# Optimization experiments

Hardware: AMD Instinct MI355X
Metric: run time of the kernel (lower is better)

The kernel has to match this reference:

```python
import jax, jax.numpy as jnp
import numpy as np

B, C, O = 16384, 128, 128


def setup_inputs() -> dict:
    key = jax.random.key(0)
    k1, k2, k3 = jax.random.split(key, 3)
    x = jax.random.normal(k1, (B, C, 3, 3), dtype=jnp.float32)
    # 9 stacked Conv2d(C, O, 3x3) weights/biases, position p = 3*r + c (row-major)
    W = jax.random.normal(k2, (9, O, C, 3, 3), dtype=jnp.float32) * 0.05
    b = jax.random.normal(k3, (9, O), dtype=jnp.float32) * 0.05
    return {"x": x, "W": W, "b": b}


def reference(x, W, b):
    Bn = x.shape[0]
    xr = x.reshape(Bn, C, 3, 3)
    # F.interpolate(scale_factor=3, mode='nearest'): each pixel replicated 3x3
    ins = jnp.repeat(jnp.repeat(xr, 3, axis=2), 3, axis=3)  # (B, C, 9, 9)
    # patch for output position (r, c) is ins[:, :, 2+r:5+r, 2+c:5+c]
    patches = jnp.stack(
        [ins[:, :, 2 + r:5 + r, 2 + c:5 + c] for r in range(3) for c in range(3)],
        axis=0,
    )  # (9, B, C, 3, 3)
    # each conv reduces its 3x3xC patch to one pixel per out-channel
    out = jnp.einsum('pbcij,pocij->bpo', patches, W) + b[None]  # (B, 9, O)
    out = out.transpose(0, 2, 1).reshape(Bn, O, 3, 3)  # row-major (r, c)
    return out
```

## Files before the change

kernel.cpp:

```cpp
#include <hip/hip_runtime.h>
#include <hip/hip_bf16.h>

typedef __bf16 bf16_t;
typedef __attribute__((ext_vector_type(8))) __bf16 bf16x8;
typedef __attribute__((ext_vector_type(4))) float f32x4;

#define KDIM 1152
#define NDIM 1152
#define BM 128
#define BN 288
#define BK 32
#define NIT 36
#define NTILES 4
#define A_STEP 8192
#define A_PANEL 294912
#define B_STEP 18432
#define B_TILE (36 * B_STEP)
#define CVT_BLOCKS 9216

__device__ __forceinline__ void gload_lds16(const void* g, void* l) {
    __builtin_amdgcn_global_load_lds(
        (const __attribute__((address_space(1))) void*)g,
        (__attribute__((address_space(3))) void*)l, 16, 0, 0);
}

__global__ void prep(const float* __restrict__ X, bf16_t* __restrict__ Xb,
                     const float* __restrict__ W, const float* __restrict__ bvec,
                     bf16_t* __restrict__ Bm, float* __restrict__ bias)
{
    __shared__ char L[4096];
    const int bid = blockIdx.x;
    const int tid = threadIdx.x;
    if (bid < CVT_BLOCKS) {
        const int wv = (bid << 2) + (tid >> 6);
        const int l = tid & 63;
        const int P = wv / 288;
        const int rem = wv - P * 288;
        const int T = rem >> 3;
        const int rb = rem & 7;
        const int row = P * 128 + rb * 16 + (l >> 2);
        const int k = T * 32 + (l & 3) * 8;
        const float* src = X + (size_t)row * KDIM + k;
        f32x4 lo = *(const f32x4*)src;
        f32x4 hi = *(const f32x4*)(src + 4);
        bf16x8 v;
        #pragma unroll
        for (int e = 0; e < 4; ++e) { v[e] = (__bf16)lo[e]; v[4 + e] = (__bf16)hi[e]; }
        char* wl = L + (tid >> 6) * 1024;
        *(bf16x8*)(wl + ((l & 3) * 16 + (l >> 2)) * 16) = v;
        __builtin_amdgcn_s_barrier();
        bf16x8 o = *(const bf16x8*)(wl + l * 16);
        *(bf16x8*)((char*)Xb + ((size_t)wv * 64 + l) * 16) = o;
        return;
    }
    const int t = (bid - CVT_BLOCKS) * 256 + tid;
    if (t < NDIM) {
        const int o = t / 9, p = t - o * 9;
        bias[t] = bvec[p * 128 + o];
    }
    const int c = t & 127;
    const int o = (t >> 7) & 127;
    const int p = t >> 14;
    if (p >= 9) return;
    const int r = p / 3, cc = p - r * 3;
    float eff[3][3] = {{0.f,0.f,0.f},{0.f,0.f,0.f},{0.f,0.f,0.f}};
    const float* w = W + (size_t)((p * 128 + o) * 128 + c) * 9;
    #pragma unroll
    for (int i = 0; i < 3; ++i) {
        const int a = (2 + r + i) / 3;
        #pragma unroll
        for (int j = 0; j < 3; ++j) {
            const int bb = (2 + cc + j) / 3;
            eff[a][bb] += w[i * 3 + j];
        }
    }
    const int n = o * 9 + p;
    const int tile = n / BN;
    const int nin = n - tile * BN;
    #pragma unroll
    for (int a = 0; a < 3; ++a)
        #pragma unroll
        for (int bb = 0; bb < 3; ++bb) {
            const int k = c * 9 + a * 3 + bb;
            const size_t idx = (size_t)tile * (B_TILE / 2)
                             + (k >> 5) * (B_STEP / 2)
                             + (nin >> 4) * 512 + ((k >> 3) & 3) * 128
                             + (nin & 15) * 8 + (k & 7);
            Bm[idx] = (bf16_t)eff[a][bb];
        }
}

__launch_bounds__(256, 2)
__global__ void ind_gemm(const bf16_t* __restrict__ Xb,
                         const bf16_t* __restrict__ Bm,
                         const float* __restrict__ bias,
                         float* __restrict__ out)
{
    __shared__ char As[2][A_STEP];
    __shared__ char Bs[2][B_STEP];
    __shared__ char Scrap[1024];

    const int tid = threadIdx.x;
    const int lane = tid & 63;
    const int wid = tid >> 6;
    const int wm = wid >> 1;
    const int wn = wid & 1;

    const int bid = blockIdx.x;
    const int swz = (bid & 7) * 64 + (bid >> 3);
    const int mt = swz >> 2;
    const int nt = swz & 3;
    const int m0 = mt * BM;

    const int fr = (lane >> 4) * 256 + (lane & 15) * 16;
    const char* apanel = (const char*)Xb + (size_t)mt * A_PANEL;
    const char* bpanel = (const char*)Bm + (size_t)nt * B_TILE;

    f32x4 acc[4][9];
    #pragma unroll
    for (int i = 0; i < 4; ++i)
        #pragma unroll
        for (int j = 0; j < 9; ++j)
            acc[i][j] = (f32x4){0.f, 0.f, 0.f, 0.f};

    bf16x8 af[4], bfr[9];

    #define GLD(T, BUF) do {                                                \
        const char* sa_ = apanel + (size_t)(T) * A_STEP;                    \
        gload_lds16(sa_ + tid * 16,        &As[BUF][tid * 16]);             \
        gload_lds16(sa_ + 4096 + tid * 16, &As[BUF][4096 + tid * 16]);      \
        const char* sb_ = bpanel + (size_t)(T) * B_STEP;                    \
        _Pragma("unroll")                                                   \
        for (int r_ = 0; r_ < 4; ++r_) {                                    \
            const int u_ = (tid + r_ * 256) * 16;                           \
            gload_lds16(sb_ + u_, &Bs[BUF][u_]);                            \
        }                                                                   \
        if (tid < 128) gload_lds16(sb_ + (1024 + tid) * 16,                 \
                                   &Bs[BUF][(1024 + tid) * 16]);            \
        else           gload_lds16(bpanel + tid * 16, Scrap);               \
    } while (0)

    #define RD(CUR) do {                                                    \
        _Pragma("unroll")                                                   \
        for (int mi_ = 0; mi_ < 4; ++mi_)                                   \
            af[mi_] = *(const bf16x8*)(&As[CUR][(wm * 4 + mi_) * 1024 + fr]); \
        _Pragma("unroll")                                                   \
        for (int j_ = 0; j_ < 9; ++j_)                                      \
            bfr[j_] = *(const bf16x8*)(&Bs[CUR][(wn * 9 + j_) * 1024 + fr]); \
        asm volatile("s_waitcnt lgkmcnt(0)" ::: "memory");                  \
        __builtin_amdgcn_sched_barrier(0);                                  \
        __builtin_amdgcn_s_barrier();                                       \
    } while (0)

    #define MFMA36() do {                                                   \
        __builtin_amdgcn_s_setprio(1);                                      \
        _Pragma("unroll")                                                   \
        for (int mi_ = 0; mi_ < 4; ++mi_)                                   \
            _Pragma("unroll")                                               \
            for (int j_ = 0; j_ < 9; ++j_)                                  \
                acc[mi_][j_] = __builtin_amdgcn_mfma_f32_16x16x32_bf16(     \
                    af[mi_], bfr[j_], acc[mi_][j_], 0, 0, 0);               \
        __builtin_amdgcn_s_setprio(0);                                      \
    } while (0)

    #define WAITV(N) do {                                                   \
        asm volatile("s_waitcnt vmcnt(" #N ")" ::: "memory");               \
        __builtin_amdgcn_sched_barrier(0);                                  \
    } while (0)

    GLD(0, 0);
    GLD(1, 1);
    WAITV(7);
    __builtin_amdgcn_s_barrier();

    #pragma unroll 1
    for (int t2 = 0; t2 < 17; ++t2) {
        const int t = 2 * t2;
        RD(0);
        GLD(t + 2, 0);
        MFMA36();
        WAITV(7);
        __builtin_amdgcn_s_barrier();
        RD(1);
        GLD(t + 3, 1);
        MFMA36();
        WAITV(7);
        __builtin_amdgcn_s_barrier();
    }
    RD(0);
    MFMA36();
    WAITV(0);
    __builtin_amdgcn_s_barrier();
    RD(1);
    MFMA36();

    #undef GLD
    #undef RD
    #undef MFMA36
    #undef WAITV

    const int orow = (lane >> 4) * 4;
    const int ocol = lane & 15;
    const int gn0 = nt * BN + wn * 144 + ocol;
    #pragma unroll
    for (int ni = 0; ni < 9; ++ni) {
        const float bv = bias[gn0 + ni * 16];
        #pragma unroll
        for (int mi = 0; mi < 4; ++mi) {
            float* po = out + (size_t)(m0 + wm * 64 + mi * 16 + orow) * NDIM
                            + gn0 + ni * 16;
            #pragma unroll
            for (int r = 0; r < 4; ++r)
                po[(size_t)r * NDIM] = acc[mi][ni][r] + bv;
        }
    }
}

extern "C" void kernel_launch(void* const* d_in, const int* in_sizes, int n_in,
                              void* d_out, int out_size, void* d_ws, size_t ws_size,
                              hipStream_t stream)
{
    const float* x  = (const float*)d_in[0];
    const float* W  = (const float*)d_in[1];
    const float* bv = (const float*)d_in[2];
    float* out = (float*)d_out;

    bf16_t* Xb   = (bf16_t*)d_ws;
    bf16_t* Bm   = (bf16_t*)((char*)d_ws + (size_t)16384 * KDIM * sizeof(bf16_t));
    float*  bias = (float*)((char*)Bm + (size_t)KDIM * NDIM * sizeof(bf16_t));

    prep<<<CVT_BLOCKS + 576, 256, 0, stream>>>(x, Xb, W, bv, Bm, bias);
    ind_gemm<<<512, 256, 0, stream>>>(Xb, Bm, bias, out);
}
```

Baseline: 79.98 us.

## Triple-buffer GEMM LDS stages and double work per prep convert block

The GEMM main loop moves from double to triple LDS buffering. Each iteration now issues the load for stage t+2 into a third slot before reading the current slot, and one of the two barriers per step is removed. This is meant to hide global-load latency and cut synchronisation. Separately, the bf16 convert blocks in prep each handle two 16x32 tiles per wave, halving the block count. The larger LDS footprint (about 79KB per block) may reduce occupancy under the two-blocks-per-CU launch bound.

```diff
diff --git a/kernel.cpp b/kernel.cpp
--- a/kernel.cpp
+++ b/kernel.cpp
@@ -16,7 +16,7 @@
 #define A_PANEL 294912
 #define B_STEP 18432
 #define B_TILE (36 * B_STEP)
-#define CVT_BLOCKS 9216
+#define CVT_BLOCKS 4608
 
 __device__ __forceinline__ void gload_lds16(const void* g, void* l) {
     __builtin_amdgcn_global_load_lds(
@@ -28,29 +28,50 @@
                      const float* __restrict__ W, const float* __restrict__ bvec,
                      bf16_t* __restrict__ Bm, float* __restrict__ bias)
 {
-    __shared__ char L[4096];
+    __shared__ char L[8192];
     const int bid = blockIdx.x;
     const int tid = threadIdx.x;
     if (bid < CVT_BLOCKS) {
-        const int wv = (bid << 2) + (tid >> 6);
+        const int gv = (bid << 3) + ((tid >> 6) << 1);
         const int l = tid & 63;
-        const int P = wv / 288;
-        const int rem = wv - P * 288;
-        const int T = rem >> 3;
-        const int rb = rem & 7;
-        const int row = P * 128 + rb * 16 + (l >> 2);
-        const int k = T * 32 + (l & 3) * 8;
-        const float* src = X + (size_t)row * KDIM + k;
-        f32x4 lo = *(const f32x4*)src;
-        f32x4 hi = *(const f32x4*)(src + 4);
-        bf16x8 v;
-        #pragma unroll
-        for (int e = 0; e < 4; ++e) { v[e] = (__bf16)lo[e]; v[4 + e] = (__bf16)hi[e]; }
-        char* wl = L + (tid >> 6) * 1024;
-        *(bf16x8*)(wl + ((l & 3) * 16 + (l >> 2)) * 16) = v;
+        char* wl = L + (tid >> 6) * 2048;
+        {
+            const int P = gv / 288;
+            const int rem = gv - P * 288;
+            const int T = rem >> 3;
+            const int rb = rem & 7;
+            const int row = P * 128 + rb * 16 + (l >> 2);
+            const int k = T * 32 + (l & 3) * 8;
+            const float* src = X + (size_t)row * KDIM + k;
+            f32x4 lo = *(const f32x4*)src;
+            f32x4 hi = *(const f32x4*)(src + 4);
+            bf16x8 v;
+            #pragma unroll
+            for (int e = 0; e < 4; ++e) { v[e] = (__bf16)lo[e]; v[4 + e] = (__bf16)hi[e]; }
+            *(bf16x8*)(wl + ((l & 3) * 16 + (l >> 2)) * 16) = v;
+        }
+        {
+            const int g1 = gv + 1;
+            const int P = g1 / 288;
+            const int rem = g1 - P * 288;
+            const int T = rem >> 3;
+            const int rb = rem & 7;
+            const int row = P * 128 + rb * 16 + (l >> 2);
+            const int k = T * 32 + (l & 3) * 8;
+            const float* src = X + (size_t)row * KDIM + k;
+            f32x4 lo = *(const f32x4*)src;
+            f32x4 hi = *(const f32x4*)(src + 4);
+            bf16x8 v;
+            #pragma unroll
+            for (int e = 0; e < 4; ++e) { v[e] = (__bf16)lo[e]; v[4 + e] = (__bf16)hi[e]; }
+            *(bf16x8*)(wl + 1024 + ((l & 3) * 16 + (l >> 2)) * 16) = v;
+        }
         __builtin_amdgcn_s_barrier();
-        bf16x8 o = *(const bf16x8*)(wl + l * 16);
-        *(bf16x8*)((char*)Xb + ((size_t)wv * 64 + l) * 16) = o;
+        bf16x8 o0 = *(const bf16x8*)(wl + l * 16);
+        bf16x8 o1 = *(const bf16x8*)(wl + 1024 + l * 16);
+        char* dst = (char*)Xb + (size_t)gv * 1024;
+        *(bf16x8*)(dst + l * 16) = o0;
+        *(bf16x8*)(dst + 1024 + l * 16) = o1;
         return;
     }
     const int t = (bid - CVT_BLOCKS) * 256 + tid;
@@ -96,8 +117,8 @@
                          const float* __restrict__ bias,
                          float* __restrict__ out)
 {
-    __shared__ char As[2][A_STEP];
-    __shared__ char Bs[2][B_STEP];
+    __shared__ char As[3][A_STEP];
+    __shared__ char Bs[3][B_STEP];
     __shared__ char Scrap[1024];
 
     const int tid = threadIdx.x;
@@ -125,31 +146,30 @@
 
     bf16x8 af[4], bfr[9];
 
-    #define GLD(T, BUF) do {                                                \
+    #define GLD(T, SLOT) do {                                               \
         const char* sa_ = apanel + (size_t)(T) * A_STEP;                    \
-        gload_lds16(sa_ + tid * 16,        &As[BUF][tid * 16]);             \
-        gload_lds16(sa_ + 4096 + tid * 16, &As[BUF][4096 + tid * 16]);      \
+        gload_lds16(sa_ + tid * 16,        &As[SLOT][tid * 16]);            \
+        gload_lds16(sa_ + 4096 + tid * 16, &As[SLOT][4096 + tid * 16]);     \
         const char* sb_ = bpanel + (size_t)(T) * B_STEP;                    \
         _Pragma("unroll")                                                   \
         for (int r_ = 0; r_ < 4; ++r_) {                                    \
             const int u_ = (tid + r_ * 256) * 16;                           \
-            gload_lds16(sb_ + u_, &Bs[BUF][u_]);                            \
+            gload_lds16(sb_ + u_, &Bs[SLOT][u_]);                           \
         }                                                                   \
         if (tid < 128) gload_lds16(sb_ + (1024 + tid) * 16,                 \
-                                   &Bs[BUF][(1024 + tid) * 16]);            \
+                                   &Bs[SLOT][(1024 + tid) * 16]);           \
         else           gload_lds16(bpanel + tid * 16, Scrap);               \
     } while (0)
 
-    #define RD(CUR) do {                                                    \
+    #define RD(SLOT) do {                                                   \
         _Pragma("unroll")                                                   \
         for (int mi_ = 0; mi_ < 4; ++mi_)                                   \
-            af[mi_] = *(const bf16x8*)(&As[CUR][(wm * 4 + mi_) * 1024 + fr]); \
+            af[mi_] = *(const bf16x8*)(&As[SLOT][(wm * 4 + mi_) * 1024 + fr]); \
         _Pragma("unroll")                                                   \
         for (int j_ = 0; j_ < 9; ++j_)                                      \
-            bfr[j_] = *(const bf16x8*)(&Bs[CUR][(wn * 9 + j_) * 1024 + fr]); \
+            bfr[j_] = *(const bf16x8*)(&Bs[SLOT][(wn * 9 + j_) * 1024 + fr]); \
         asm volatile("s_waitcnt lgkmcnt(0)" ::: "memory");                  \
         __builtin_amdgcn_sched_barrier(0);                                  \
-        __builtin_amdgcn_s_barrier();                                       \
     } while (0)
 
     #define MFMA36() do {                                                   \
@@ -168,36 +188,39 @@
         __builtin_amdgcn_sched_barrier(0);                                  \
     } while (0)
 
+    #define ITER(T, SLOT, SLOT2) do {                                       \
+        GLD((T) + 2, SLOT2);      \
+        RD(SLOT);                                                           \
+        MFMA36();                                                           \
+        WAITV(7);                      \
+        __builtin_amdgcn_s_barrier();                                       \
+    } while (0)
+
     GLD(0, 0);
     GLD(1, 1);
     WAITV(7);
     __builtin_amdgcn_s_barrier();
 
     #pragma unroll 1
-    for (int t2 = 0; t2 < 17; ++t2) {
-        const int t = 2 * t2;
-        RD(0);
-        GLD(t + 2, 0);
-        MFMA36();
-        WAITV(7);
-        __builtin_amdgcn_s_barrier();
-        RD(1);
-        GLD(t + 3, 1);
-        MFMA36();
-        WAITV(7);
-        __builtin_amdgcn_s_barrier();
-    }
-    RD(0);
+    for (int tt = 0; tt < 11; ++tt) {
+        const int t = 3 * tt;
+        ITER(t,     0, 2);
+        ITER(t + 1, 1, 0);
+        ITER(t + 2, 2, 1);
+    }
+    ITER(33, 0, 2);
+    RD(1);
     MFMA36();
     WAITV(0);
     __builtin_amdgcn_s_barrier();
-    RD(1);
+    RD(2);
     MFMA36();
 
     #undef GLD
     #undef RD
     #undef MFMA36
     #undef WAITV
+    #undef ITER
 
     const int orow = (lane >> 4) * 4;
     const int ocol = lane & 15;
```

After: 85.82 us. 1.07x slower.

## Fuse fp32-to-bf16 activation conversion into GEMM, loading raw fp32 tiles to LDS

Applied to the files above, without the earlier changes.

Removes the separate pass that converted X to bf16 into a tiled workspace layout. The GEMM now streams fp32 X rows directly into LDS with an XOR swizzle and converts to bf16 in registers just before the MFMAs. This saves a full write and re-read of the converted activation, but doubles the A-tile LDS footprint and global bytes the GEMM loads. It also adds conversion instructions to the MFMA loop.

```diff
diff --git a/kernel.cpp b/kernel.cpp
--- a/kernel.cpp
+++ b/kernel.cpp
@@ -12,11 +12,9 @@
 #define BK 32
 #define NIT 36
 #define NTILES 4
-#define A_STEP 8192
-#define A_PANEL 294912
+#define AF_STEP 16384
 #define B_STEP 18432
 #define B_TILE (36 * B_STEP)
-#define CVT_BLOCKS 9216
 
 __device__ __forceinline__ void gload_lds16(const void* g, void* l) {
     __builtin_amdgcn_global_load_lds(
@@ -24,36 +22,12 @@
         (__attribute__((address_space(3))) void*)l, 16, 0, 0);
 }
 
-__global__ void prep(const float* __restrict__ X, bf16_t* __restrict__ Xb,
-                     const float* __restrict__ W, const float* __restrict__ bvec,
-                     bf16_t* __restrict__ Bm, float* __restrict__ bias)
+__global__ void build_wb(const float* __restrict__ W,
+                         const float* __restrict__ bvec,
+                         bf16_t* __restrict__ Bm,
+                         float* __restrict__ bias)
 {
-    __shared__ char L[4096];
-    const int bid = blockIdx.x;
-    const int tid = threadIdx.x;
-    if (bid < CVT_BLOCKS) {
-        const int wv = (bid << 2) + (tid >> 6);
-        const int l = tid & 63;
-        const int P = wv / 288;
-        const int rem = wv - P * 288;
-        const int T = rem >> 3;
-        const int rb = rem & 7;
-        const int row = P * 128 + rb * 16 + (l >> 2);
-        const int k = T * 32 + (l & 3) * 8;
-        const float* src = X + (size_t)row * KDIM + k;
-        f32x4 lo = *(const f32x4*)src;
-        f32x4 hi = *(const f32x4*)(src + 4);
-        bf16x8 v;
-        #pragma unroll
-        for (int e = 0; e < 4; ++e) { v[e] = (__bf16)lo[e]; v[4 + e] = (__bf16)hi[e]; }
-        char* wl = L + (tid >> 6) * 1024;
-        *(bf16x8*)(wl + ((l & 3) * 16 + (l >> 2)) * 16) = v;
-        __builtin_amdgcn_s_barrier();
-        bf16x8 o = *(const bf16x8*)(wl + l * 16);
-        *(bf16x8*)((char*)Xb + ((size_t)wv * 64 + l) * 16) = o;
-        return;
-    }
-    const int t = (bid - CVT_BLOCKS) * 256 + tid;
+    const int t = blockIdx.x * blockDim.x + threadIdx.x;
     if (t < NDIM) {
         const int o = t / 9, p = t - o * 9;
         bias[t] = bvec[p * 128 + o];
@@ -91,12 +65,12 @@
 }
 
 __launch_bounds__(256, 2)
-__global__ void ind_gemm(const bf16_t* __restrict__ Xb,
+__global__ void ind_gemm(const float* __restrict__ X,
                          const bf16_t* __restrict__ Bm,
                          const float* __restrict__ bias,
                          float* __restrict__ out)
 {
-    __shared__ char As[2][A_STEP];
+    __shared__ char Af[2][AF_STEP];
     __shared__ char Bs[2][B_STEP];
     __shared__ char Scrap[1024];
 
@@ -112,8 +86,16 @@
     const int nt = swz & 3;
     const int m0 = mt * BM;
 
+    const int row0 = tid >> 3;
+    const int kb0 = (tid & 7) ^ (row0 & 7);
+    const char* asrc = (const char*)(X + (size_t)(m0 + row0) * KDIM + kb0 * 4);
+
+    const int abase = (wm * 64 + (lane & 15)) * 128;
+    const int g2 = (lane >> 4) * 2;
+    const int x0 = ((g2)     ^ (lane & 7)) * 16;
+    const int x1 = ((g2 + 1) ^ (lane & 7)) * 16;
+
     const int fr = (lane >> 4) * 256 + (lane & 15) * 16;
-    const char* apanel = (const char*)Xb + (size_t)mt * A_PANEL;
     const char* bpanel = (const char*)Bm + (size_t)nt * B_TILE;
 
     f32x4 acc[4][9];
@@ -123,12 +105,15 @@
         for (int j = 0; j < 9; ++j)
             acc[i][j] = (f32x4){0.f, 0.f, 0.f, 0.f};
 
-    bf16x8 af[4], bfr[9];
+    f32x4 alo[4], ahi[4];
+    bf16x8 bfr[9];
 
     #define GLD(T, BUF) do {                                                \
-        const char* sa_ = apanel + (size_t)(T) * A_STEP;                    \
-        gload_lds16(sa_ + tid * 16,        &As[BUF][tid * 16]);             \
-        gload_lds16(sa_ + 4096 + tid * 16, &As[BUF][4096 + tid * 16]);      \
+        const char* sa_ = asrc + (size_t)(T) * 128;                         \
+        _Pragma("unroll")                                                   \
+        for (int r_ = 0; r_ < 4; ++r_)                                      \
+            gload_lds16(sa_ + (size_t)r_ * 147456,                          \
+                        &Af[BUF][tid * 16 + r_ * 4096]);                    \
         const char* sb_ = bpanel + (size_t)(T) * B_STEP;                    \
         _Pragma("unroll")                                                   \
         for (int r_ = 0; r_ < 4; ++r_) {                                    \
@@ -142,8 +127,10 @@
 
     #define RD(CUR) do {                                                    \
         _Pragma("unroll")                                                   \
-        for (int mi_ = 0; mi_ < 4; ++mi_)                                   \
-            af[mi_] = *(const bf16x8*)(&As[CUR][(wm * 4 + mi_) * 1024 + fr]); \
+        for (int mi_ = 0; mi_ < 4; ++mi_) {                                 \
+            alo[mi_] = *(const f32x4*)(&Af[CUR][abase + mi_ * 2048 + x0]);  \
+            ahi[mi_] = *(const f32x4*)(&Af[CUR][abase + mi_ * 2048 + x1]);  \
+        }                                                                   \
         _Pragma("unroll")                                                   \
         for (int j_ = 0; j_ < 9; ++j_)                                      \
             bfr[j_] = *(const bf16x8*)(&Bs[CUR][(wn * 9 + j_) * 1024 + fr]); \
@@ -155,11 +142,18 @@
     #define MFMA36() do {                                                   \
         __builtin_amdgcn_s_setprio(1);                                      \
         _Pragma("unroll")                                                   \
-        for (int mi_ = 0; mi_ < 4; ++mi_)                                   \
+        for (int mi_ = 0; mi_ < 4; ++mi_) {                                 \
+            bf16x8 a_;                                                      \
+            _Pragma("unroll")                                               \
+            for (int e_ = 0; e_ < 4; ++e_) {                                \
+                a_[e_]     = (__bf16)alo[mi_][e_];                          \
+                a_[4 + e_] = (__bf16)ahi[mi_][e_];                          \
+            }                                                               \
             _Pragma("unroll")                                               \
             for (int j_ = 0; j_ < 9; ++j_)                                  \
                 acc[mi_][j_] = __builtin_amdgcn_mfma_f32_16x16x32_bf16(     \
-                    af[mi_], bfr[j_], acc[mi_][j_], 0, 0, 0);               \
+                    a_, bfr[j_], acc[mi_][j_], 0, 0, 0);                    \
+        }                                                                   \
         __builtin_amdgcn_s_setprio(0);                                      \
     } while (0)
 
@@ -170,7 +164,7 @@
 
     GLD(0, 0);
     GLD(1, 1);
-    WAITV(7);
+    WAITV(9);
     __builtin_amdgcn_s_barrier();
 
     #pragma unroll 1
@@ -179,12 +173,12 @@
         RD(0);
         GLD(t + 2, 0);
         MFMA36();
-        WAITV(7);
+        WAITV(9);
         __builtin_amdgcn_s_barrier();
         RD(1);
         GLD(t + 3, 1);
         MFMA36();
-        WAITV(7);
+        WAITV(9);
         __builtin_amdgcn_s_barrier();
     }
     RD(0);
@@ -225,10 +219,9 @@
     const float* bv = (const float*)d_in[2];
     float* out = (float*)d_out;
 
-    bf16_t* Xb   = (bf16_t*)d_ws;
-    bf16_t* Bm   = (bf16_t*)((char*)d_ws + (size_t)16384 * KDIM * sizeof(bf16_t));
-    float*  bias = (float*)((char*)Bm + (size_t)KDIM * NDIM * sizeof(bf16_t));
-
-    prep<<<CVT_BLOCKS + 576, 256, 0, stream>>>(x, Xb, W, bv, Bm, bias);
-    ind_gemm<<<512, 256, 0, stream>>>(Xb, Bm, bias, out);
-}
+    bf16_t* Bm   = (bf16_t*)d_ws;
+    float*  bias = (float*)((char*)d_ws + (size_t)KDIM * NDIM * sizeof(bf16_t));
+
+    build_wb<<<576, 256, 0, stream>>>(W, bv, Bm, bias);
+    ind_gemm<<<512, 256, 0, stream>>>(x, Bm, bias, out);
+}
```

Result: faster. 75.42 us (median of 5 runs) (-5.7%).
